# Performance work log

Hardware: AMD Instinct MI355X
Metric: run time of the kernel (lower is better)

Reference implementation:

```python
import jax, jax.numpy as jnp
import numpy as np

C_IN, C_OUT, K, H = 64, 128, 27, 100000

def setup_inputs() -> dict:
    key = jax.random.key(0)
    k1, k2, k3 = jax.random.split(key, 3)
    data_in = jax.random.normal(k1, (1, C_IN, H, 1), dtype=jnp.float32)
    # neighbor index table: 27 neighbors per node; -1 would mean 'missing' (zero-padded)
    neigh = jax.random.randint(k2, (H, K), 0, H, dtype=jnp.int64)
    # conv weight, fan-in scaled init, stored [C_out, C_in, K]
    weight = jax.random.normal(k3, (C_OUT, C_IN, K), dtype=jnp.float32) / np.sqrt(C_IN * K)
    return {"data_in": data_in, "neigh": neigh, "weight": weight}

def reference(data_in, neigh, weight):
    # data_in: [1, C_in, H, 1] (ocnn layout) -> [C_in, H]
    x = data_in[0, :, :, 0]
    # octree2col: gather 27 neighbors per node -> [C_in, H, K]
    cols = x[:, neigh]
    # zero out missing neighbors (index < 0)
    cols = jnp.where(neigh[None, :, :] >= 0, cols, jnp.zeros((), dtype=cols.dtype))
    # GEMM over (C_in, K) fused with ReLU -> [C_out, H]
    out = jnp.einsum('chk,ock->oh', cols, weight)
    out = jax.nn.relu(out)
    return out[None, :, :, None]  # back to ocnn layout [1, C_out, H, 1]
```

## Files before the change

kernel.cpp:

```cpp
#include <hip/hip_runtime.h>
#include <hip/hip_bf16.h>

#define C_IN  64
#define C_OUT 128
#define KK    27
#define HH    100000
#define TB    1563
#define WB    108
#define NBLK  391

typedef __attribute__((ext_vector_type(8))) short s8v;
typedef __attribute__((ext_vector_type(4))) float f32x4;

__device__ inline unsigned short f2bf(float f) {
    __hip_bfloat16 h = __float2bfloat16(f);
    return *reinterpret_cast<unsigned short*>(&h);
}

__device__ inline void dma16(const void* g, void* l) {
    __builtin_amdgcn_global_load_lds((const __attribute__((address_space(1))) void*)g,
                                     (__attribute__((address_space(3))) void*)l, 16, 0, 0);
}

__global__ __launch_bounds__(256) void prep_kernel(const float* __restrict__ x,
                                                   const float* __restrict__ w,
                                                   unsigned short* __restrict__ xt,
                                                   unsigned short* __restrict__ wk) {
    const int tid = threadIdx.x;
    if (blockIdx.x < TB) {
        __shared__ __align__(16) unsigned short ts[64 * 72];
        const int hbase = blockIdx.x * 64;
        #pragma unroll
        for (int it = 0; it < 16; ++it) {
            int i = it * 256 + tid;
            int c = i >> 6, hl = i & 63;
            int hg = hbase + hl;
            float v = (hg < HH) ? x[(size_t)c * HH + hg] : 0.f;
            ts[hl * 72 + c] = f2bf(v);
        }
        __syncthreads();
        #pragma unroll
        for (int it = 0; it < 2; ++it) {
            int u = it * 256 + tid;
            int hl = u >> 3, part = u & 7;
            int hg = hbase + hl;
            if (hg < HH)
                *(int4*)&xt[(size_t)hg * 64 + part * 8] = *(const int4*)&ts[hl * 72 + part * 8];
        }
    } else {
        int b = blockIdx.x - TB;
        int base = b * 2048 + tid;
        #pragma unroll
        for (int j = 0; j < 8; ++j) {
            int t = base + j * 256;
            int jj = t & 63, o = (t >> 6) & 127, kx = t >> 13;
            int lc = (jj >> 3) ^ (o & 7);
            int c  = lc * 8 + (jj & 7);
            wk[t] = f2bf(w[(size_t)o * (C_IN * KK) + c * KK + kx]);
        }
    }
}

__global__ __launch_bounds__(256, 2) void conv_main(const unsigned short* __restrict__ xt,
                                                    const unsigned short* __restrict__ wk,
                                                    const int* __restrict__ neigh,
                                                    float* __restrict__ out) {
    __shared__ int neigh_s[256 * KK];
    __shared__ __align__(16) unsigned short w_s[2][128 * 64];

    const int tid  = threadIdx.x;
    const int wave = tid >> 6;
    const int lane = tid & 63;
    const int col  = lane & 15;
    const int quad = lane >> 4;
    const int hbase = blockIdx.x * 256;

    #pragma unroll
    for (int j = 0; j < KK; ++j) {
        int i = j * 256 + tid;
        int hl = i / KK, kx = i - hl * KK;
        int hg = hbase + hl;
        neigh_s[i] = (hg < HH) ? neigh[(size_t)hg * KK + kx] : -1;
    }

    {
        const unsigned short* src = wk;
        #pragma unroll
        for (int i = 0; i < 4; ++i) {
            int row_base = wave * 8 + i * 32;
            dma16(src + row_base * 64 + lane * 8, &w_s[0][row_base * 64]);
        }
    }

    f32x4 acc[8][4];
    #pragma unroll
    for (int mt = 0; mt < 8; ++mt)
        #pragma unroll
        for (int nt = 0; nt < 4; ++nt)
            acc[mt][nt] = (f32x4){0.f, 0.f, 0.f, 0.f};

    __syncthreads();

    int4 cur[2][4], nxt[2][4];
    const int pc_b = (quad * 8);
    auto loadB = [&](int kk, int4 (&frag)[2][4]) {
        #pragma unroll
        for (int nt = 0; nt < 4; ++nt) {
            int n = wave * 64 + nt * 16 + col;
            int idx = neigh_s[n * KK + kk];
            if (idx >= 0) {
                const unsigned short* base = xt + (size_t)idx * 64 + pc_b;
                frag[0][nt] = *(const int4*)(base);
                frag[1][nt] = *(const int4*)(base + 32);
            } else {
                frag[0][nt] = make_int4(0, 0, 0, 0);
                frag[1][nt] = make_int4(0, 0, 0, 0);
            }
        }
    };

    loadB(0, cur);

    int p = 0;
    #pragma unroll 1
    for (int k = 0; k < KK; ++k) {
        if (k + 1 < KK) {
            const unsigned short* src = wk + (size_t)(k + 1) * (C_OUT * C_IN);
            #pragma unroll
            for (int i = 0; i < 4; ++i) {
                int row_base = wave * 8 + i * 32;
                dma16(src + row_base * 64 + lane * 8, &w_s[p ^ 1][row_base * 64]);
            }
            loadB(k + 1, nxt);
        }

        #pragma unroll
        for (int ch = 0; ch < 2; ++ch) {
            const int pc = (ch * 4 + quad) ^ (col & 7);
            #pragma unroll
            for (int mt = 0; mt < 8; ++mt) {
                s8v a = *(const s8v*)&w_s[p][(mt * 16 + col) * 64 + pc * 8];
                #pragma unroll
                for (int nt = 0; nt < 4; ++nt) {
                    s8v b = __builtin_bit_cast(s8v, cur[ch][nt]);
                    acc[mt][nt] = __builtin_amdgcn_mfma_f32_16x16x32_bf16(a, b, acc[mt][nt], 0, 0, 0);
                }
            }
        }

        __syncthreads();
        #pragma unroll
        for (int ch = 0; ch < 2; ++ch)
            #pragma unroll
            for (int nt = 0; nt < 4; ++nt)
                cur[ch][nt] = nxt[ch][nt];
        p ^= 1;
    }

    #pragma unroll
    for (int mt = 0; mt < 8; ++mt) {
        #pragma unroll
        for (int nt = 0; nt < 4; ++nt) {
            int hg = hbase + wave * 64 + nt * 16 + col;
            if (hg < HH) {
                #pragma unroll
                for (int r = 0; r < 4; ++r) {
                    int o = mt * 16 + quad * 4 + r;
                    float v = acc[mt][nt][r];
                    out[(size_t)o * HH + hg] = v > 0.f ? v : 0.f;
                }
            }
        }
    }
}

extern "C" void kernel_launch(void* const* d_in, const int* in_sizes, int n_in,
                              void* d_out, int out_size, void* d_ws, size_t ws_size,
                              hipStream_t stream) {
    const float* data_in = (const float*)d_in[0];
    const int*   neigh   = (const int*)d_in[1];
    const float* weight  = (const float*)d_in[2];
    float* out = (float*)d_out;

    unsigned short* xt = (unsigned short*)d_ws;
    unsigned short* wk = xt + (size_t)HH * 64;

    prep_kernel<<<TB + WB, 256, 0, stream>>>(data_in, weight, xt, wk);
    conv_main<<<NBLK, 256, 0, stream>>>(xt, wk, neigh, out);
}
```

Measured before the change: 166.7 us.

## Branchless neighbor gather via zero row, unrolled double-buffer, finer waitcnt barrier

Adds a zeroed sentinel row at index HH in the transposed input buffer so missing neighbors load from it, which removes the per-fragment branch. The main loop is unrolled by two with ping-pong fragment registers, so the register copies of nxt into cur go away. The full __syncthreads is replaced by a partial vmcnt wait plus s_barrier, so the next fragment loads can stay in flight across the barrier. The weight DMA and first-neighbor gathers are also issued before the neighbor table is staged in LDS. The hand-written waitcnt assumes a particular count of outstanding loads, which carries a correctness risk for the LDS DMA ordering.

```diff
diff --git a/kernel.cpp b/kernel.cpp
--- a/kernel.cpp
+++ b/kernel.cpp
@@ -49,6 +49,8 @@
         }
     } else {
         int b = blockIdx.x - TB;
+        if (b == 0 && tid < 64)
+            *(int4*)&xt[(size_t)HH * 64 + tid * 8] = make_int4(0, 0, 0, 0);
         int base = b * 2048 + tid;
         #pragma unroll
         for (int j = 0; j < 8; ++j) {
@@ -76,20 +78,31 @@
     const int hbase = blockIdx.x * 256;
 
     #pragma unroll
+    for (int i = 0; i < 4; ++i) {
+        int row_base = wave * 8 + i * 32;
+        dma16(wk + row_base * 64 + lane * 8, &w_s[0][row_base * 64]);
+    }
+
+    int4 b0[2][4], b1[2][4];
+    {
+        #pragma unroll
+        for (int nt = 0; nt < 4; ++nt) {
+            int n  = wave * 64 + nt * 16 + col;
+            int hg = hbase + n;
+            int idx = (hg < HH) ? neigh[(size_t)hg * KK] : -1;
+            int idxc = (idx < 0) ? HH : idx;
+            const unsigned short* base = xt + (size_t)idxc * 64 + quad * 8;
+            b0[0][nt] = *(const int4*)(base);
+            b0[1][nt] = *(const int4*)(base + 32);
+        }
+    }
+
+    #pragma unroll
     for (int j = 0; j < KK; ++j) {
         int i = j * 256 + tid;
         int hl = i / KK, kx = i - hl * KK;
         int hg = hbase + hl;
         neigh_s[i] = (hg < HH) ? neigh[(size_t)hg * KK + kx] : -1;
-    }
-
-    {
-        const unsigned short* src = wk;
-        #pragma unroll
-        for (int i = 0; i < 4; ++i) {
-            int row_base = wave * 8 + i * 32;
-            dma16(src + row_base * 64 + lane * 8, &w_s[0][row_base * 64]);
-        }
     }
 
     f32x4 acc[8][4];
@@ -101,45 +114,37 @@
 
     __syncthreads();
 
-    int4 cur[2][4], nxt[2][4];
-    const int pc_b = (quad * 8);
     auto loadB = [&](int kk, int4 (&frag)[2][4]) {
         #pragma unroll
         for (int nt = 0; nt < 4; ++nt) {
             int n = wave * 64 + nt * 16 + col;
             int idx = neigh_s[n * KK + kk];
-            if (idx >= 0) {
-                const unsigned short* base = xt + (size_t)idx * 64 + pc_b;
-                frag[0][nt] = *(const int4*)(base);
-                frag[1][nt] = *(const int4*)(base + 32);
-            } else {
-                frag[0][nt] = make_int4(0, 0, 0, 0);
-                frag[1][nt] = make_int4(0, 0, 0, 0);
-            }
+            int idxc = (idx < 0) ? HH : idx;
+            const unsigned short* base = xt + (size_t)idxc * 64 + quad * 8;
+            frag[0][nt] = *(const int4*)(base);
+            frag[1][nt] = *(const int4*)(base + 32);
         }
     };
 
-    loadB(0, cur);
-
-    int p = 0;
-    #pragma unroll 1
-    for (int k = 0; k < KK; ++k) {
-        if (k + 1 < KK) {
+    auto step = [&](int k, int4 (&cur)[2][4], int4 (&nxt)[2][4], bool last) {
+        if (!last) {
             const unsigned short* src = wk + (size_t)(k + 1) * (C_OUT * C_IN);
+            unsigned short* dst = &w_s[(k + 1) & 1][0];
             #pragma unroll
             for (int i = 0; i < 4; ++i) {
                 int row_base = wave * 8 + i * 32;
-                dma16(src + row_base * 64 + lane * 8, &w_s[p ^ 1][row_base * 64]);
+                dma16(src + row_base * 64 + lane * 8, dst + row_base * 64);
             }
             loadB(k + 1, nxt);
         }
 
+        const unsigned short* wp = &w_s[k & 1][0];
         #pragma unroll
         for (int ch = 0; ch < 2; ++ch) {
             const int pc = (ch * 4 + quad) ^ (col & 7);
             #pragma unroll
             for (int mt = 0; mt < 8; ++mt) {
-                s8v a = *(const s8v*)&w_s[p][(mt * 16 + col) * 64 + pc * 8];
+                s8v a = *(const s8v*)&wp[(mt * 16 + col) * 64 + pc * 8];
                 #pragma unroll
                 for (int nt = 0; nt < 4; ++nt) {
                     s8v b = __builtin_bit_cast(s8v, cur[ch][nt]);
@@ -148,14 +153,18 @@
             }
         }
 
-        __syncthreads();
-        #pragma unroll
-        for (int ch = 0; ch < 2; ++ch)
-            #pragma unroll
-            for (int nt = 0; nt < 4; ++nt)
-                cur[ch][nt] = nxt[ch][nt];
-        p ^= 1;
+        if (!last) {
+            asm volatile("s_waitcnt vmcnt(8) lgkmcnt(0)" ::: "memory");
+            __builtin_amdgcn_s_barrier();
+        }
+    };
+
+    #pragma unroll 1
+    for (int k = 0; k < KK - 1; k += 2) {
+        step(k,     b0, b1, false);
+        step(k + 1, b1, b0, false);
     }
+    step(KK - 1, b0, b1, true);
 
     #pragma unroll
     for (int mt = 0; mt < 8; ++mt) {
@@ -183,7 +192,7 @@
     float* out = (float*)d_out;
 
     unsigned short* xt = (unsigned short*)d_ws;
-    unsigned short* wk = xt + (size_t)HH * 64;
+    unsigned short* wk = xt + (size_t)(HH + 8) * 64;
 
     prep_kernel<<<TB + WB, 256, 0, stream>>>(data_in, weight, xt, wk);
     conv_main<<<NBLK, 256, 0, stream>>>(xt, wk, neigh, out);
```

After: 168.4 us. Within noise of the previous version (+1.0%).
